# Optimization experiments

Hardware: AMD Instinct MI355X
Metric: run time of the kernel (lower is better)

Reference implementation:

```python
import jax, jax.numpy as jnp
import numpy as np

K = 7            # kernel_size (odd)
R = K // 2       # neighborhood radius
NH = 16          # num_heads


def _starts(L):
    """NATTEN (dilation=1) window start and rpb start per query index."""
    i = jnp.arange(L)
    win = jnp.clip(i - R, 0, L - K)  # key-window start (window clamped inside image)
    pb = jnp.where(i < R, 2 * R - i, jnp.where(i + R >= L, L - 1 - i, R))
    return win, pb


def setup_inputs() -> dict:
    key = jax.random.key(0)
    ks = jax.random.split(key, 12)
    B, H, W, C = 2, 128, 128, 512
    std = 0.02
    return {
        "q": jax.random.normal(ks[0], (B, H, W, C), jnp.float32),
        "k": jax.random.normal(ks[1], (B, H, W, C), jnp.float32),
        "v": jax.random.normal(ks[2], (B, H, W, C), jnp.float32),
        "wq": jax.random.normal(ks[3], (C, C), jnp.float32) * std,
        "bq": jnp.zeros((C,), jnp.float32),
        "wk": jax.random.normal(ks[4], (C, C), jnp.float32) * std,
        "bk": jnp.zeros((C,), jnp.float32),
        "wv": jax.random.normal(ks[5], (C, C), jnp.float32) * std,
        "bv": jnp.zeros((C,), jnp.float32),
        "rpb": jax.random.normal(ks[6], (NH, 2 * K - 1, 2 * K - 1), jnp.float32) * std,
        "wo": jax.random.normal(ks[7], (C, C), jnp.float32) * std,
        "bo": jnp.zeros((C,), jnp.float32),
    }


def reference(q, k, v, wq, bq, wk, bk, wv, bv, rpb, wo, bo):
    B, H, W, C = q.shape
    hd = C // NH
    scale = hd ** -0.5

    def proj(x, w, b):
        y = x @ w.T + b  # torch nn.Linear
        return y.reshape(B, H, W, NH, hd).transpose(0, 3, 1, 2, 4)  # [B,nh,H,W,hd]

    qh = proj(q, wq, bq) * scale
    kh = proj(k, wk, bk)
    vh = proj(v, wv, bv)

    # H,W (128) >= window_size (7): torch padding branch is dead and omitted.
    sh, ph = _starts(H)
    sw, pw = _starts(W)

    # natten2dqkrpb: per-offset shifted-row/col gathers; never materialize
    # the dense [B,nh,H,W,k*k,hd] unfold.
    logits = []
    for a in range(K):
        kh_a = kh[:, :, sh + a]          # [B,nh,H,W,hd]
        rpb_a = rpb[:, ph + a]           # [nh,H,2K-1]
        for b in range(K):
            k_ab = kh_a[:, :, :, sw + b]             # [B,nh,H,W,hd]
            bias = rpb_a[:, :, pw + b]               # [nh,H,W]
            logits.append(jnp.einsum("bnhwd,bnhwd->bnhw", qh, k_ab) + bias[None])
    attn = jax.nn.softmax(jnp.stack(logits, axis=-1), axis=-1)  # [B,nh,H,W,K*K]

    # natten2dav
    x = jnp.zeros_like(qh)
    for a in range(K):
        vh_a = vh[:, :, sh + a]
        for b in range(K):
            v_ab = vh_a[:, :, :, sw + b]
            x = x + attn[..., a * K + b, None] * v_ab

    x = x.transpose(0, 2, 3, 1, 4).reshape(B, H, W, C)
    return x @ wo.T + bo
```

## Files before the change

### kernel.cpp

```cpp
#include <hip/hip_runtime.h>
#include <hip/hip_bf16.h>

typedef __attribute__((ext_vector_type(8))) short          s16x8;
typedef __attribute__((ext_vector_type(8))) unsigned short u16x8;
typedef __attribute__((ext_vector_type(4))) float          f4;
typedef __attribute__((ext_vector_type(2))) float          f2;
typedef __attribute__((ext_vector_type(4))) unsigned int   u32x4;

__device__ __forceinline__ float bf2f(unsigned short u) {
    union { unsigned int i; float f; } x; x.i = ((unsigned int)u) << 16; return x.f;
}
__device__ __forceinline__ float blo(unsigned int w) {
    union { unsigned int i; float f; } x; x.i = w << 16; return x.f;
}
__device__ __forceinline__ float bhi(unsigned int w) {
    union { unsigned int i; float f; } x; x.i = w & 0xffff0000u; return x.f;
}
__device__ __forceinline__ unsigned short f2bf(float f) {
    __hip_bfloat16 h = __float2bfloat16(f);
    return *reinterpret_cast<unsigned short*>(&h);
}
__device__ __forceinline__ void gload_lds16(const void* g, void* l) {
    __builtin_amdgcn_global_load_lds(
        (const __attribute__((address_space(1))) unsigned int*)g,
        (__attribute__((address_space(3))) unsigned int*)l, 16, 0, 0);
}

__global__ __launch_bounds__(256) void cvt_w4(const float* __restrict__ a,
                                              const float* __restrict__ b,
                                              const float* __restrict__ c,
                                              const float* __restrict__ d,
                                              unsigned short* __restrict__ o) {
    const int i   = (blockIdx.x * 256 + threadIdx.x) * 8;
    const int seg = i >> 18;
    const int off = i & 262143;
    const float* s = (seg == 0) ? a : (seg == 1) ? b : (seg == 2) ? c : d;
    f4 x0 = *(const f4*)(s + off);
    f4 x1 = *(const f4*)(s + off + 4);
    unsigned short t[8];
    t[0] = f2bf(x0[0]); t[1] = f2bf(x0[1]); t[2] = f2bf(x0[2]); t[3] = f2bf(x0[3]);
    t[4] = f2bf(x1[0]); t[5] = f2bf(x1[1]); t[6] = f2bf(x1[2]); t[7] = f2bf(x1[3]);
    *(u16x8*)(o + i) = *(u16x8*)t;
}

template <bool AF32, bool OF32>
__global__ __launch_bounds__(256, 2) void gemm_fn(const void* __restrict__ Ap,
                                                  const unsigned short* __restrict__ Wb,
                                                  const float* __restrict__ bias,
                                                  void* __restrict__ Outp,
                                                  float scale) {
    constexpr int KD = 512, BK = 32, NT = KD / BK;
    constexpr int ASZ = AF32 ? 64 * BK * 4 : 64 * BK * 2;
    constexpr int WSZ = 512 * BK * 2;
    constexpr int STRIDE = ASZ + WSZ;
    extern __shared__ unsigned char lds[];

    const int tid  = threadIdx.x;
    const int lane = tid & 63;
    const int w    = tid >> 6;
    const size_t m0 = (size_t)blockIdx.x * 64;

    const float*          Af = (const float*)Ap;
    const unsigned short* Ab = (const unsigned short*)Ap;

    const int fr = lane & 15;
    const int j4 = lane >> 4;

    f4 acc[4][8];
#pragma unroll
    for (int i = 0; i < 4; ++i)
#pragma unroll
        for (int j = 0; j < 8; ++j) acc[i][j] = (f4)(0.0f);

    auto stage = [&](int t, int buf) {
        const int kt = t * BK;
        unsigned char* base = lds + buf * STRIDE;
        if constexpr (AF32) {
#pragma unroll
            for (int i = 0; i < 2; ++i) {
                const int f = i * 256 + tid;
                const int row = f >> 3, p = f & 7;
                const int s = p ^ (row & 7);
                gload_lds16(Af + (m0 + row) * KD + kt + s * 4, base + f * 16);
            }
        } else {
            const int f = tid;
            const int l = f ^ ((f >> 3) & 7);
            gload_lds16(Ab + (m0 + (l >> 2)) * KD + kt + (l & 3) * 8, base + f * 16);
        }
#pragma unroll
        for (int i = 0; i < 8; ++i) {
            const int f = i * 256 + tid;
            const int l = f ^ ((f >> 3) & 7);
            gload_lds16(Wb + (size_t)(l >> 2) * KD + kt + (l & 3) * 8,
                        base + ASZ + f * 16);
        }
    };

    stage(0, 0);
    stage(1, 1);

    for (int t = 0; t < NT; ++t) {
        const int buf = t & 1;
        unsigned char* base = lds + buf * STRIDE;
        if (t + 1 < NT) {
            if constexpr (AF32) asm volatile("s_waitcnt vmcnt(10)" ::: "memory");
            else                asm volatile("s_waitcnt vmcnt(9)"  ::: "memory");
        } else {
            asm volatile("s_waitcnt vmcnt(0)" ::: "memory");
        }
        __builtin_amdgcn_s_barrier();
        __builtin_amdgcn_sched_barrier(0);

        s16x8 af[4];
#pragma unroll
        for (int mi = 0; mi < 4; ++mi) {
            const int row = mi * 16 + fr;
            if constexpr (AF32) {
                const int r7 = row & 7;
                const int s0 = j4 * 2;
                f4 x0 = *(const f4*)(base + row * 128 + ((s0 ^ r7) << 4));
                f4 x1 = *(const f4*)(base + row * 128 + (((s0 + 1) ^ r7) << 4));
                unsigned short u[8];
                u[0] = f2bf(x0[0]); u[1] = f2bf(x0[1]); u[2] = f2bf(x0[2]); u[3] = f2bf(x0[3]);
                u[4] = f2bf(x1[0]); u[5] = f2bf(x1[1]); u[6] = f2bf(x1[2]); u[7] = f2bf(x1[3]);
                af[mi] = *(s16x8*)u;
            } else {
                const int L = (row << 2) | j4;
                const int P = L ^ ((L >> 3) & 7);
                af[mi] = *(const s16x8*)(base + (P << 4));
            }
        }
#pragma unroll
        for (int ni = 0; ni < 8; ++ni) {
            const int nrow = w * 128 + ni * 16 + fr;
            const int L = (nrow << 2) | j4;
            const int P = L ^ ((L >> 3) & 7);
            const s16x8 bf = *(const s16x8*)(base + ASZ + (P << 4));
#pragma unroll
            for (int mi = 0; mi < 4; ++mi)
                acc[mi][ni] = __builtin_amdgcn_mfma_f32_16x16x32_bf16(
                    af[mi], bf, acc[mi][ni], 0, 0, 0);
        }

        __builtin_amdgcn_sched_barrier(0);
        __builtin_amdgcn_s_barrier();
        __builtin_amdgcn_sched_barrier(0);
        if (t + 2 < NT) stage(t + 2, buf);
    }

    const int rq = (lane >> 4) << 2;
#pragma unroll
    for (int ni = 0; ni < 8; ++ni) {
        const int   col = w * 128 + ni * 16 + fr;
        const float bv  = bias[col];
#pragma unroll
        for (int mi = 0; mi < 4; ++mi) {
            const size_t rbase = m0 + mi * 16 + rq;
#pragma unroll
            for (int r = 0; r < 4; ++r) {
                const float val = (acc[mi][ni][r] + bv) * scale;
                if constexpr (OF32)
                    ((float*)Outp)[(rbase + r) * KD + col] = val;
                else
                    ((unsigned short*)Outp)[(rbase + r) * KD + col] = f2bf(val);
            }
        }
    }
}

__global__ __launch_bounds__(256, 4) void natt(const unsigned short* __restrict__ qh,
                                               const unsigned short* __restrict__ kh,
                                               const unsigned short* __restrict__ vh,
                                               const float* __restrict__ rpb,
                                               unsigned short* __restrict__ xout) {
    constexpr int LDK = 40;
    __shared__ unsigned short KV[484][LDK];
    __shared__ float Rs[169];

    const int tid = threadIdx.x;
    const int h   = blockIdx.z & 15;
    const int b   = blockIdx.z >> 4;
    const int x0  = blockIdx.x * 16;
    const int y0  = blockIdx.y * 16;
    const int ux0 = min(max(x0 - 3, 0), 106);
    const int uy0 = min(max(y0 - 3, 0), 106);
    const int tx  = tid & 15;
    const int ty  = tid >> 4;
    const int x   = x0 + tx;
    const int y   = y0 + ty;

    if (tid < 169) Rs[tid] = rpb[h * 169 + tid];

    const long imgbase = (long)b * 128 * 128;

#pragma unroll 2
    for (int kk = tid; kk < 484; kk += 256) {
        const int ky = uy0 + kk / 22;
        const int kx = ux0 + kk % 22;
        const unsigned short* src = kh + (imgbase + ky * 128 + kx) * 512 + h * 32;
#pragma unroll
        for (int j = 0; j < 4; ++j)
            *(u16x8*)&KV[kk][j * 8] = *(const u16x8*)(src + j * 8);
    }

    const long pix = imgbase + y * 128 + x;
    const unsigned short* qp = qh + pix * 512 + h * 32;
    f2 qv[16];
#pragma unroll
    for (int j = 0; j < 4; ++j) {
        u16x8 v = *(const u16x8*)(qp + j * 8);
#pragma unroll
        for (int e = 0; e < 4; ++e)
            qv[j * 4 + e] = (f2){bf2f(v[2 * e]), bf2f(v[2 * e + 1])};
    }

    const int myy = min(max(y - 3, 0), 121) - uy0;
    const int myx = min(max(x - 3, 0), 121) - ux0;
    const int pbY = (y < 3) ? (6 - y) : ((y >= 125) ? (127 - y) : 3);
    const int pbX = (x < 3) ? (6 - x) : ((x >= 125) ? (127 - x) : 3);

    __syncthreads();

    float logit[49];
#pragma unroll
    for (int a = 0; a < 7; ++a) {
        const int rowk = (myy + a) * 22 + myx;
#pragma unroll
        for (int c = 0; c < 7; ++c) {
            const u32x4* kp = (const u32x4*)&KV[rowk + c][0];
            f2 sA = {0.f, 0.f}, sB = {0.f, 0.f};
#pragma unroll
            for (int j = 0; j < 4; ++j) {
                const u32x4 w = kp[j];
                sA += qv[4 * j + 0] * (f2){blo(w[0]), bhi(w[0])};
                sB += qv[4 * j + 1] * (f2){blo(w[1]), bhi(w[1])};
                sA += qv[4 * j + 2] * (f2){blo(w[2]), bhi(w[2])};
                sB += qv[4 * j + 3] * (f2){blo(w[3]), bhi(w[3])};
            }
            logit[a * 7 + c] = (sA[0] + sA[1]) + (sB[0] + sB[1])
                             + Rs[(pbY + a) * 13 + pbX + c];
        }
    }

    float m = logit[0];
#pragma unroll
    for (int i = 1; i < 49; ++i) m = fmaxf(m, logit[i]);
    float sum = 0.f;
#pragma unroll
    for (int i = 0; i < 49; ++i) {
        float p = exp2f((logit[i] - m) * 1.4426950408889634f);
        logit[i] = p;
        sum += p;
    }
    const float rinv = 1.f / sum;
#pragma unroll
    for (int i = 0; i < 49; ++i) logit[i] *= rinv;

    __syncthreads();

#pragma unroll 2
    for (int kk = tid; kk < 484; kk += 256) {
        const int ky = uy0 + kk / 22;
        const int kx = ux0 + kk % 22;
        const unsigned short* src = vh + (imgbase + ky * 128 + kx) * 512 + h * 32;
#pragma unroll
        for (int j = 0; j < 4; ++j)
            *(u16x8*)&KV[kk][j * 8] = *(const u16x8*)(src + j * 8);
    }
    __syncthreads();

    f2 acc2[16];
#pragma unroll
    for (int d = 0; d < 16; ++d) acc2[d] = (f2){0.f, 0.f};
#pragma unroll
    for (int a = 0; a < 7; ++a) {
        const int rowk = (myy + a) * 22 + myx;
#pragma unroll
        for (int c = 0; c < 7; ++c) {
            const u32x4* vp = (const u32x4*)&KV[rowk + c][0];
            const float wgt = logit[a * 7 + c];
            const f2 w2 = {wgt, wgt};
#pragma unroll
            for (int j = 0; j < 4; ++j) {
                const u32x4 w = vp[j];
                acc2[4 * j + 0] += w2 * (f2){blo(w[0]), bhi(w[0])};
                acc2[4 * j + 1] += w2 * (f2){blo(w[1]), bhi(w[1])};
                acc2[4 * j + 2] += w2 * (f2){blo(w[2]), bhi(w[2])};
                acc2[4 * j + 3] += w2 * (f2){blo(w[3]), bhi(w[3])};
            }
        }
    }

    unsigned short* op = xout + pix * 512 + h * 32;
#pragma unroll
    for (int j = 0; j < 4; ++j) {
        unsigned short t[8];
#pragma unroll
        for (int e = 0; e < 4; ++e) {
            t[2 * e]     = f2bf(acc2[j * 4 + e][0]);
            t[2 * e + 1] = f2bf(acc2[j * 4 + e][1]);
        }
        *(u16x8*)(op + j * 8) = *(u16x8*)t;
    }
}

extern "C" void kernel_launch(void* const* d_in, const int* in_sizes, int n_in,
                              void* d_out, int out_size, void* d_ws, size_t ws_size,
                              hipStream_t stream) {
    const float* q   = (const float*)d_in[0];
    const float* k   = (const float*)d_in[1];
    const float* v   = (const float*)d_in[2];
    const float* wq  = (const float*)d_in[3];
    const float* bq  = (const float*)d_in[4];
    const float* wk  = (const float*)d_in[5];
    const float* bk  = (const float*)d_in[6];
    const float* wv  = (const float*)d_in[7];
    const float* bv  = (const float*)d_in[8];
    const float* rpb = (const float*)d_in[9];
    const float* wo  = (const float*)d_in[10];
    const float* bo  = (const float*)d_in[11];

    const long P = 2l * 128 * 128;
    unsigned short* qh = (unsigned short*)d_ws;
    unsigned short* kh = qh + P * 512;
    unsigned short* vh = kh + P * 512;
    unsigned short* xb = vh + P * 512;
    unsigned short* Wb = xb + P * 512;

    const float scale = 0.17677669529663687f;
    const size_t smemF = 2 * (64 * 32 * 4 + 512 * 32 * 2);
    const size_t smemB = 2 * (64 * 32 * 2 + 512 * 32 * 2);

    cvt_w4<<<512, 256, 0, stream>>>(wq, wk, wv, wo, Wb);

    gemm_fn<true, false><<<512, 256, smemF, stream>>>(q, Wb,          bq, qh, scale);
    gemm_fn<true, false><<<512, 256, smemF, stream>>>(k, Wb + 262144, bk, kh, 1.0f);
    gemm_fn<true, false><<<512, 256, smemF, stream>>>(v, Wb + 524288, bv, vh, 1.0f);

    natt<<<dim3(8, 8, 32), 256, 0, stream>>>(qh, kh, vh, rpb, xb);

    gemm_fn<false, true><<<512, 256, smemB, stream>>>(xb, Wb + 786432, bo, (float*)d_out, 1.0f);
}
```

Measured before the change: 256.1 us.

## Use head-major q/k/v/x layout and preload full fp32 A panel in projection GEMMs

Intermediate q/k/v/x buffers move from pixel-major [pix][512] to head-major [head][pix][32], so each attention block gathers contiguous 64-byte rows per head. The projection GEMM now loads the whole 64x512 fp32 activation panel into registers up front and converts it to bf16 once into padded LDS. Only the weights stream through double-buffered LDS, and MFMA operands are swapped to produce a transposed tile that matches the new store layout. The output GEMM becomes its own kernel that reads the head-major x buffer. This costs extra registers (128 floats per thread for the preload) and LDS, which may lower occupancy.

```diff
diff --git a/kernel.cpp b/kernel.cpp
--- a/kernel.cpp
+++ b/kernel.cpp
@@ -6,6 +6,9 @@
 typedef __attribute__((ext_vector_type(4))) float          f4;
 typedef __attribute__((ext_vector_type(2))) float          f2;
 typedef __attribute__((ext_vector_type(4))) unsigned int   u32x4;
+typedef __attribute__((ext_vector_type(2))) unsigned int   u32x2;
+
+#define NPIX 32768
 
 __device__ __forceinline__ float bf2f(unsigned short u) {
     union { unsigned int i; float f; } x; x.i = ((unsigned int)u) << 16; return x.f;
@@ -19,6 +22,9 @@
 __device__ __forceinline__ unsigned short f2bf(float f) {
     __hip_bfloat16 h = __float2bfloat16(f);
     return *reinterpret_cast<unsigned short*>(&h);
+}
+__device__ __forceinline__ unsigned int pk2(float a, float b) {
+    return (unsigned int)f2bf(a) | ((unsigned int)f2bf(b) << 16);
 }
 __device__ __forceinline__ void gload_lds16(const void* g, void* l) {
     __builtin_amdgcn_global_load_lds(
@@ -43,128 +49,199 @@
     *(u16x8*)(o + i) = *(u16x8*)t;
 }
 
-template <bool AF32, bool OF32>
-__global__ __launch_bounds__(256, 2) void gemm_fn(const void* __restrict__ Ap,
-                                                  const unsigned short* __restrict__ Wb,
-                                                  const float* __restrict__ bias,
-                                                  void* __restrict__ Outp,
-                                                  float scale) {
-    constexpr int KD = 512, BK = 32, NT = KD / BK;
-    constexpr int ASZ = AF32 ? 64 * BK * 4 : 64 * BK * 2;
-    constexpr int WSZ = 512 * BK * 2;
-    constexpr int STRIDE = ASZ + WSZ;
+__global__ __launch_bounds__(256) void gemm_proj(const float* __restrict__ Af,
+                                                 const unsigned short* __restrict__ Wb,
+                                                 const float* __restrict__ bias,
+                                                 unsigned short* __restrict__ Out,
+                                                 float scale) {
+    constexpr int AP = 1040;
+    constexpr int ASZ = 64 * AP;
+    constexpr int WSZ = 512 * 32 * 2;
     extern __shared__ unsigned char lds[];
+    unsigned char* Wl = lds + ASZ;
 
     const int tid  = threadIdx.x;
     const int lane = tid & 63;
     const int w    = tid >> 6;
+    const int fr   = lane & 15;
+    const int j4   = lane >> 4;
     const size_t m0 = (size_t)blockIdx.x * 64;
-
-    const float*          Af = (const float*)Ap;
-    const unsigned short* Ab = (const unsigned short*)Ap;
-
-    const int fr = lane & 15;
-    const int j4 = lane >> 4;
-
-    f4 acc[4][8];
-#pragma unroll
-    for (int i = 0; i < 4; ++i)
-#pragma unroll
-        for (int j = 0; j < 8; ++j) acc[i][j] = (f4)(0.0f);
-
-    auto stage = [&](int t, int buf) {
-        const int kt = t * BK;
-        unsigned char* base = lds + buf * STRIDE;
-        if constexpr (AF32) {
-#pragma unroll
-            for (int i = 0; i < 2; ++i) {
-                const int f = i * 256 + tid;
-                const int row = f >> 3, p = f & 7;
-                const int s = p ^ (row & 7);
-                gload_lds16(Af + (m0 + row) * KD + kt + s * 4, base + f * 16);
-            }
-        } else {
-            const int f = tid;
-            const int l = f ^ ((f >> 3) & 7);
-            gload_lds16(Ab + (m0 + (l >> 2)) * KD + kt + (l & 3) * 8, base + f * 16);
-        }
+    const float* panel = Af + m0 * 512;
+
+    f4 av[32];
+#pragma unroll
+    for (int i = 0; i < 32; ++i)
+        av[i] = *(const f4*)((const unsigned char*)panel + i * 4096 + tid * 16);
+
+    auto stageW = [&](int t) {
+        unsigned char* base = Wl + (t & 1) * WSZ;
+        const int kt = t * 32;
 #pragma unroll
         for (int i = 0; i < 8; ++i) {
             const int f = i * 256 + tid;
             const int l = f ^ ((f >> 3) & 7);
-            gload_lds16(Wb + (size_t)(l >> 2) * KD + kt + (l & 3) * 8,
-                        base + ASZ + f * 16);
+            gload_lds16(Wb + (size_t)(l >> 2) * 512 + kt + (l & 3) * 8,
+                        base + f * 16);
         }
     };
-
-    stage(0, 0);
-    stage(1, 1);
-
-    for (int t = 0; t < NT; ++t) {
-        const int buf = t & 1;
-        unsigned char* base = lds + buf * STRIDE;
-        if (t + 1 < NT) {
-            if constexpr (AF32) asm volatile("s_waitcnt vmcnt(10)" ::: "memory");
-            else                asm volatile("s_waitcnt vmcnt(9)"  ::: "memory");
-        } else {
-            asm volatile("s_waitcnt vmcnt(0)" ::: "memory");
-        }
+    stageW(0);
+    stageW(1);
+
+#pragma unroll
+    for (int i = 0; i < 32; ++i) {
+        const int idx = i * 1024 + tid * 4;
+        const int row = idx >> 9;
+        const int k   = idx & 511;
+        u32x2 p;
+        p[0] = pk2(av[i][0], av[i][1]);
+        p[1] = pk2(av[i][2], av[i][3]);
+        *(u32x2*)(lds + row * AP + k * 2) = p;
+    }
+    __syncthreads();
+
+    f4 acc[4][8];
+#pragma unroll
+    for (int i = 0; i < 4; ++i)
+#pragma unroll
+        for (int j = 0; j < 8; ++j) acc[i][j] = (f4)(0.0f);
+
+    for (int t = 0; t < 16; ++t) {
+        if (t < 15) asm volatile("s_waitcnt vmcnt(8)" ::: "memory");
+        else        asm volatile("s_waitcnt vmcnt(0)" ::: "memory");
         __builtin_amdgcn_s_barrier();
         __builtin_amdgcn_sched_barrier(0);
 
-        s16x8 af[4];
-#pragma unroll
-        for (int mi = 0; mi < 4; ++mi) {
-            const int row = mi * 16 + fr;
-            if constexpr (AF32) {
-                const int r7 = row & 7;
-                const int s0 = j4 * 2;
-                f4 x0 = *(const f4*)(base + row * 128 + ((s0 ^ r7) << 4));
-                f4 x1 = *(const f4*)(base + row * 128 + (((s0 + 1) ^ r7) << 4));
-                unsigned short u[8];
-                u[0] = f2bf(x0[0]); u[1] = f2bf(x0[1]); u[2] = f2bf(x0[2]); u[3] = f2bf(x0[3]);
-                u[4] = f2bf(x1[0]); u[5] = f2bf(x1[1]); u[6] = f2bf(x1[2]); u[7] = f2bf(x1[3]);
-                af[mi] = *(s16x8*)u;
-            } else {
-                const int L = (row << 2) | j4;
-                const int P = L ^ ((L >> 3) & 7);
-                af[mi] = *(const s16x8*)(base + (P << 4));
-            }
-        }
-#pragma unroll
-        for (int ni = 0; ni < 8; ++ni) {
-            const int nrow = w * 128 + ni * 16 + fr;
-            const int L = (nrow << 2) | j4;
+        unsigned char* wbase = Wl + (t & 1) * WSZ;
+        s16x8 wf[8], af[4];
+#pragma unroll
+        for (int ct = 0; ct < 8; ++ct) {
+            const int c = w * 128 + ct * 16 + fr;
+            const int L = (c << 2) | j4;
             const int P = L ^ ((L >> 3) & 7);
-            const s16x8 bf = *(const s16x8*)(base + ASZ + (P << 4));
-#pragma unroll
-            for (int mi = 0; mi < 4; ++mi)
-                acc[mi][ni] = __builtin_amdgcn_mfma_f32_16x16x32_bf16(
-                    af[mi], bf, acc[mi][ni], 0, 0, 0);
-        }
+            wf[ct] = *(const s16x8*)(wbase + (P << 4));
+        }
+#pragma unroll
+        for (int pt = 0; pt < 4; ++pt)
+            af[pt] = *(const s16x8*)(lds + (pt * 16 + fr) * AP + t * 64 + j4 * 16);
+#pragma unroll
+        for (int pt = 0; pt < 4; ++pt)
+#pragma unroll
+            for (int ct = 0; ct < 8; ++ct)
+                acc[pt][ct] = __builtin_amdgcn_mfma_f32_16x16x32_bf16(
+                    wf[ct], af[pt], acc[pt][ct], 0, 0, 0);
 
         __builtin_amdgcn_sched_barrier(0);
         __builtin_amdgcn_s_barrier();
         __builtin_amdgcn_sched_barrier(0);
-        if (t + 2 < NT) stage(t + 2, buf);
-    }
-
-    const int rq = (lane >> 4) << 2;
-#pragma unroll
-    for (int ni = 0; ni < 8; ++ni) {
-        const int   col = w * 128 + ni * 16 + fr;
-        const float bv  = bias[col];
-#pragma unroll
-        for (int mi = 0; mi < 4; ++mi) {
-            const size_t rbase = m0 + mi * 16 + rq;
-#pragma unroll
-            for (int r = 0; r < 4; ++r) {
-                const float val = (acc[mi][ni][r] + bv) * scale;
-                if constexpr (OF32)
-                    ((float*)Outp)[(rbase + r) * KD + col] = val;
-                else
-                    ((unsigned short*)Outp)[(rbase + r) * KD + col] = f2bf(val);
-            }
+        if (t + 2 < 16) stageW(t + 2);
+    }
+
+#pragma unroll
+    for (int ct = 0; ct < 8; ++ct) {
+        const int c0 = w * 128 + ct * 16 + j4 * 4;
+        const f4 b4 = *(const f4*)(bias + c0);
+        const int h = c0 >> 5;
+        const int d = c0 & 31;
+#pragma unroll
+        for (int pt = 0; pt < 4; ++pt) {
+            const size_t pix = m0 + pt * 16 + fr;
+            const f4 v = acc[pt][ct];
+            u32x2 p;
+            p[0] = pk2((v[0] + b4[0]) * scale, (v[1] + b4[1]) * scale);
+            p[1] = pk2((v[2] + b4[2]) * scale, (v[3] + b4[3]) * scale);
+            *(u32x2*)(Out + ((size_t)h * NPIX + pix) * 32 + d) = p;
+        }
+    }
+}
+
+__global__ __launch_bounds__(256, 2) void gemm_out(const unsigned short* __restrict__ Xb,
+                                                   const unsigned short* __restrict__ Wb,
+                                                   const float* __restrict__ bias,
+                                                   float* __restrict__ Out) {
+    constexpr int XSZ = 4096, WSZ = 32768;
+    extern __shared__ unsigned char lds[];
+    unsigned char* Wl = lds + 2 * XSZ;
+
+    const int tid  = threadIdx.x;
+    const int lane = tid & 63;
+    const int w    = tid >> 6;
+    const int fr   = lane & 15;
+    const int j4   = lane >> 4;
+    const size_t m0 = (size_t)blockIdx.x * 64;
+
+    auto stageX = [&](int t) {
+        const int f = tid;
+        const int l = f ^ ((f >> 3) & 7);
+        gload_lds16(Xb + ((size_t)t * NPIX + m0 + (l >> 2)) * 32 + (l & 3) * 8,
+                    lds + (t & 1) * XSZ + f * 16);
+    };
+    auto stageW = [&](int t) {
+        unsigned char* base = Wl + (t & 1) * WSZ;
+        const int kt = t * 32;
+#pragma unroll
+        for (int i = 0; i < 8; ++i) {
+            const int f = i * 256 + tid;
+            const int l = f ^ ((f >> 3) & 7);
+            gload_lds16(Wb + (size_t)(l >> 2) * 512 + kt + (l & 3) * 8,
+                        base + f * 16);
+        }
+    };
+
+    stageX(0); stageW(0);
+    stageX(1); stageW(1);
+    __syncthreads();
+
+    f4 acc[4][8];
+#pragma unroll
+    for (int i = 0; i < 4; ++i)
+#pragma unroll
+        for (int j = 0; j < 8; ++j) acc[i][j] = (f4)(0.0f);
+
+    for (int t = 0; t < 16; ++t) {
+        if (t < 15) asm volatile("s_waitcnt vmcnt(9)" ::: "memory");
+        else        asm volatile("s_waitcnt vmcnt(0)" ::: "memory");
+        __builtin_amdgcn_s_barrier();
+        __builtin_amdgcn_sched_barrier(0);
+
+        unsigned char* xbase = lds + (t & 1) * XSZ;
+        unsigned char* wbase = Wl + (t & 1) * WSZ;
+        s16x8 af[4], wf[8];
+#pragma unroll
+        for (int pt = 0; pt < 4; ++pt) {
+            const int L = ((pt * 16 + fr) << 2) | j4;
+            const int P = L ^ ((L >> 3) & 7);
+            af[pt] = *(const s16x8*)(xbase + (P << 4));
+        }
+#pragma unroll
+        for (int ct = 0; ct < 8; ++ct) {
+            const int c = w * 128 + ct * 16 + fr;
+            const int L = (c << 2) | j4;
+            const int P = L ^ ((L >> 3) & 7);
+            wf[ct] = *(const s16x8*)(wbase + (P << 4));
+        }
+#pragma unroll
+        for (int pt = 0; pt < 4; ++pt)
+#pragma unroll
+            for (int ct = 0; ct < 8; ++ct)
+                acc[pt][ct] = __builtin_amdgcn_mfma_f32_16x16x32_bf16(
+                    af[pt], wf[ct], acc[pt][ct], 0, 0, 0);
+
+        __builtin_amdgcn_sched_barrier(0);
+        __builtin_amdgcn_s_barrier();
+        __builtin_amdgcn_sched_barrier(0);
+        if (t + 2 < 16) { stageX(t + 2); stageW(t + 2); }
+    }
+
+#pragma unroll
+    for (int ct = 0; ct < 8; ++ct) {
+        const int c = w * 128 + ct * 16 + fr;
+        const float bv = bias[c];
+#pragma unroll
+        for (int pt = 0; pt < 4; ++pt) {
+            const size_t pix = m0 + pt * 16 + j4 * 4;
+#pragma unroll
+            for (int r = 0; r < 4; ++r)
+                Out[(pix + r) * 512 + c] = acc[pt][ct][r] + bv;
         }
     }
 }
@@ -192,20 +269,20 @@
 
     if (tid < 169) Rs[tid] = rpb[h * 169 + tid];
 
-    const long imgbase = (long)b * 128 * 128;
+    const size_t hb = (size_t)h * NPIX + (size_t)b * 16384;
 
 #pragma unroll 2
     for (int kk = tid; kk < 484; kk += 256) {
         const int ky = uy0 + kk / 22;
         const int kx = ux0 + kk % 22;
-        const unsigned short* src = kh + (imgbase + ky * 128 + kx) * 512 + h * 32;
+        const unsigned short* src = kh + (hb + ky * 128 + kx) * 32;
 #pragma unroll
         for (int j = 0; j < 4; ++j)
             *(u16x8*)&KV[kk][j * 8] = *(const u16x8*)(src + j * 8);
     }
 
-    const long pix = imgbase + y * 128 + x;
-    const unsigned short* qp = qh + pix * 512 + h * 32;
+    const size_t pix = hb + y * 128 + x;
+    const unsigned short* qp = qh + pix * 32;
     f2 qv[16];
 #pragma unroll
     for (int j = 0; j < 4; ++j) {
@@ -232,11 +309,11 @@
             f2 sA = {0.f, 0.f}, sB = {0.f, 0.f};
 #pragma unroll
             for (int j = 0; j < 4; ++j) {
-                const u32x4 w = kp[j];
-                sA += qv[4 * j + 0] * (f2){blo(w[0]), bhi(w[0])};
-                sB += qv[4 * j + 1] * (f2){blo(w[1]), bhi(w[1])};
-                sA += qv[4 * j + 2] * (f2){blo(w[2]), bhi(w[2])};
-                sB += qv[4 * j + 3] * (f2){blo(w[3]), bhi(w[3])};
+                const u32x4 wv = kp[j];
+                sA += qv[4 * j + 0] * (f2){blo(wv[0]), bhi(wv[0])};
+                sB += qv[4 * j + 1] * (f2){blo(wv[1]), bhi(wv[1])};
+                sA += qv[4 * j + 2] * (f2){blo(wv[2]), bhi(wv[2])};
+                sB += qv[4 * j + 3] * (f2){blo(wv[3]), bhi(wv[3])};
             }
             logit[a * 7 + c] = (sA[0] + sA[1]) + (sB[0] + sB[1])
                              + Rs[(pbY + a) * 13 + pbX + c];
@@ -263,7 +340,7 @@
     for (int kk = tid; kk < 484; kk += 256) {
         const int ky = uy0 + kk / 22;
         const int kx = ux0 + kk % 22;
-        const unsigned short* src = vh + (imgbase + ky * 128 + kx) * 512 + h * 32;
+        const unsigned short* src = vh + (hb + ky * 128 + kx) * 32;
 #pragma unroll
         for (int j = 0; j < 4; ++j)
             *(u16x8*)&KV[kk][j * 8] = *(const u16x8*)(src + j * 8);
@@ -283,16 +360,16 @@
             const f2 w2 = {wgt, wgt};
 #pragma unroll
             for (int j = 0; j < 4; ++j) {
-                const u32x4 w = vp[j];
-                acc2[4 * j + 0] += w2 * (f2){blo(w[0]), bhi(w[0])};
-                acc2[4 * j + 1] += w2 * (f2){blo(w[1]), bhi(w[1])};
-                acc2[4 * j + 2] += w2 * (f2){blo(w[2]), bhi(w[2])};
-                acc2[4 * j + 3] += w2 * (f2){blo(w[3]), bhi(w[3])};
+                const u32x4 wv = vp[j];
+                acc2[4 * j + 0] += w2 * (f2){blo(wv[0]), bhi(wv[0])};
+                acc2[4 * j + 1] += w2 * (f2){blo(wv[1]), bhi(wv[1])};
+                acc2[4 * j + 2] += w2 * (f2){blo(wv[2]), bhi(wv[2])};
+                acc2[4 * j + 3] += w2 * (f2){blo(wv[3]), bhi(wv[3])};
             }
         }
     }
 
-    unsigned short* op = xout + pix * 512 + h * 32;
+    unsigned short* op = xout + pix * 32;
 #pragma unroll
     for (int j = 0; j < 4; ++j) {
         unsigned short t[8];
@@ -321,7 +398,7 @@
     const float* wo  = (const float*)d_in[10];
     const float* bo  = (const float*)d_in[11];
 
-    const long P = 2l * 128 * 128;
+    const long P = NPIX;
     unsigned short* qh = (unsigned short*)d_ws;
     unsigned short* kh = qh + P * 512;
     unsigned short* vh = kh + P * 512;
@@ -329,16 +406,16 @@
     unsigned short* Wb = xb + P * 512;
 
     const float scale = 0.17677669529663687f;
-    const size_t smemF = 2 * (64 * 32 * 4 + 512 * 32 * 2);
-    const size_t smemB = 2 * (64 * 32 * 2 + 512 * 32 * 2);
+    const size_t smemP = 64 * 1040 + 2 * 512 * 32 * 2;
+    const size_t smemO = 2 * 4096 + 2 * 32768;
 
     cvt_w4<<<512, 256, 0, stream>>>(wq, wk, wv, wo, Wb);
 
-    gemm_fn<true, false><<<512, 256, smemF, stream>>>(q, Wb,          bq, qh, scale);
-    gemm_fn<true, false><<<512, 256, smemF, stream>>>(k, Wb + 262144, bk, kh, 1.0f);
-    gemm_fn<true, false><<<512, 256, smemF, stream>>>(v, Wb + 524288, bv, vh, 1.0f);
+    gemm_proj<<<512, 256, smemP, stream>>>(q, Wb,          bq, qh, scale);
+    gemm_proj<<<512, 256, smemP, stream>>>(k, Wb + 262144, bk, kh, 1.0f);
+    gemm_proj<<<512, 256, smemP, stream>>>(v, Wb + 524288, bv, vh, 1.0f);
 
     natt<<<dim3(8, 8, 32), 256, 0, stream>>>(qh, kh, vh, rpb, xb);
 
-    gemm_fn<false, true><<<512, 256, smemB, stream>>>(xb, Wb + 786432, bo, (float*)d_out, 1.0f);
-}
+    gemm_out<<<512, 256, smemO, stream>>>(xb, Wb + 786432, bo, (float*)d_out);
+}
```

After: 264.9 us. 3.4% more time.
